# Optimization experiments

Measured on AMD Instinct MI355X. Metric: run time of the kernel, lower is better.

The kernel has to match this reference:

```python
import jax, jax.numpy as jnp
import numpy as np

# Module constants (from init_kwargs)
D_MODEL = 128
N_HEADS = 8
D_H = D_MODEL // N_HEADS
SCALE = D_H ** -0.5
D_IN = 8          # number of channels
SEQ_LEN = 128     # per-channel key length (S = D_IN*SEQ_LEN)


def setup_inputs() -> dict:
    key = jax.random.key(0)
    ks = jax.random.split(key, 16)
    B, P, S = 8, 512, 1024
    Q = jax.random.normal(ks[0], (B, P, D_MODEL), jnp.float32)
    K = jax.random.normal(ks[1], (B, S, D_MODEL), jnp.float32)
    V = jax.random.normal(ks[2], (B, S, D_MODEL), jnp.float32)
    prev = jax.random.normal(ks[3], (B, P, N_HEADS, S), jnp.float32)
    # cross-channel mask: attend only to tokens from a *different* channel
    pred_ch = jnp.arange(P) // (P // D_IN)          # (P,)
    seq_ch = jnp.arange(S) // SEQ_LEN               # (S,)
    attn_mask = (pred_ch[:, None] != seq_ch[None, :]).reshape(1, P, 1, S)
    w = lambda k, shp: jax.random.normal(k, shp, jnp.float32) * 0.02
    Wq, bq = w(ks[4], (D_MODEL, D_MODEL)), w(ks[5], (D_MODEL,))
    Wk, bk = w(ks[6], (D_MODEL, D_MODEL)), w(ks[7], (D_MODEL,))
    Wv, bv = w(ks[8], (D_MODEL, D_MODEL)), w(ks[9], (D_MODEL,))
    Wo, bo = w(ks[10], (D_MODEL, D_MODEL)), w(ks[11], (D_MODEL,))
    ch_gate = jax.random.normal(ks[12], (D_IN, D_IN), jnp.float32)
    return dict(Q=Q, K=K, V=V, prev=prev, attn_mask=attn_mask,
                Wq=Wq, bq=bq, Wk=Wk, bk=bk, Wv=Wv, bv=bv, Wo=Wo, bo=bo,
                ch_gate=ch_gate)


def reference(Q, K, V, prev, attn_mask, Wq, bq, Wk, bk, Wv, bv, Wo, bo, ch_gate):
    B, P, _ = Q.shape
    S = K.shape[1]
    H, dh = N_HEADS, D_H
    q = (Q @ Wq.T + bq).reshape(B, P, H, dh)
    k = (K @ Wk.T + bk).reshape(B, S, H, dh)
    v = (V @ Wv.T + bv).reshape(B, S, H, dh)
    raw_scores = jnp.einsum('bphd,bshd->bphs', q, k) * SCALE
    raw_scores = raw_scores + prev                     # residual attention
    # channel gating with STE
    pred_ch = jnp.arange(P) // (P // D_IN)
    seq_ch = jnp.arange(S) // SEQ_LEN
    s = jax.nn.sigmoid(ch_gate)
    hard = (s >= 0.5).astype(s.dtype)
    gate_ch = hard + (s - jax.lax.stop_gradient(s))
    gate_full = gate_ch[pred_ch][:, seq_ch].reshape(1, P, 1, S)
    raw_scores = jnp.where(jnp.isfinite(raw_scores), raw_scores * gate_full, raw_scores)
    # stable masked softmax with explicit renormalization
    stable = raw_scores - jnp.max(raw_scores, axis=-1, keepdims=True)
    masked = jnp.where(attn_mask, stable, -1e9)
    attn = jax.nn.softmax(masked, axis=-1)
    attn = attn * attn_mask.astype(attn.dtype)
    den = jnp.clip(jnp.sum(attn, axis=-1, keepdims=True), 1e-9, None)
    attn = attn / den
    out = jnp.einsum('bphs,bshd->bphd', attn, v).reshape(B, P, H * dh)
    out = out @ Wo.T + bo
    return out, attn, raw_scores
```

## Files before the change

kernel.cpp:

```cpp
#include <hip/hip_runtime.h>
#include <hip/hip_bf16.h>

typedef unsigned short u16;
typedef float f32x4 __attribute__((ext_vector_type(4)));
typedef __bf16 bf16x8 __attribute__((ext_vector_type(8)));
typedef _Float16 f16x8 __attribute__((ext_vector_type(8)));
typedef _Float16 f16x2 __attribute__((ext_vector_type(2)));

union Frag { int4 i; bf16x8 b; f16x8 h; };

__device__ inline u16 f2bf(float f) {
  union { float f; unsigned u; } v; v.f = f;
  unsigned r = v.u + 0x7FFFu + ((v.u >> 16) & 1u);
  return (u16)(r >> 16);
}
__device__ inline unsigned pk_f16(float a, float b) {
  return __builtin_bit_cast(unsigned, __builtin_amdgcn_cvt_pkrtz(a, b));
}

__device__ __forceinline__ void lds_barrier() {
  asm volatile("s_waitcnt lgkmcnt(0)" ::: "memory");
  __builtin_amdgcn_s_barrier();
}

__device__ __forceinline__
void proj_body(u16* __restrict__ smem,
               const float* __restrict__ X, const float* __restrict__ W,
               const float* __restrict__ bias, void* __restrict__ out,
               int mode, int innerShift, int rows0)
{
  u16* XL = smem;
  u16* WL = smem + 64 * 136;

  const int tid = threadIdx.x;
  const int w = tid >> 6, l = tid & 63, lg = l >> 4, lr = l & 15;

  #pragma unroll
  for (int i = 0; i < 8; ++i) {
    int u = tid + i * 256;
    int rr = u >> 5, c4 = (u & 31) * 4;
    const float4 xv = *(const float4*)(X + (rows0 + rr) * 128 + c4);
    uint2 p;
    p.x = (unsigned)f2bf(xv.x) | ((unsigned)f2bf(xv.y) << 16);
    p.y = (unsigned)f2bf(xv.z) | ((unsigned)f2bf(xv.w) << 16);
    *(uint2*)(XL + rr * 136 + c4) = p;
  }
  #pragma unroll
  for (int i = 0; i < 16; ++i) {
    int u = tid + i * 256;
    int rr = u >> 5, c4 = (u & 31) * 4;
    const float4 xv = *(const float4*)(W + rr * 128 + c4);
    uint2 p;
    p.x = (unsigned)f2bf(xv.x) | ((unsigned)f2bf(xv.y) << 16);
    p.y = (unsigned)f2bf(xv.z) | ((unsigned)f2bf(xv.w) << 16);
    *(uint2*)(WL + rr * 136 + c4) = p;
  }
  __syncthreads();

  Frag a[4];
  #pragma unroll
  for (int kc = 0; kc < 4; ++kc)
    a[kc].i = *(const int4*)(XL + (16 * w + lr) * 136 + kc * 32 + 8 * lg);

  f32x4 acc[8];
  #pragma unroll
  for (int ct = 0; ct < 8; ++ct) {
    f32x4 c = {0.f, 0.f, 0.f, 0.f};
    #pragma unroll
    for (int kc = 0; kc < 4; ++kc) {
      Frag bw;
      bw.i = *(const int4*)(WL + (ct * 16 + lr) * 136 + kc * 32 + 8 * lg);
      c = __builtin_amdgcn_mfma_f32_16x16x32_bf16(a[kc].b, bw.b, c, 0, 0, 0);
    }
    acc[ct] = c;
  }

  if (mode == 2) {
    float* o = (float*)out;
    #pragma unroll
    for (int ct = 0; ct < 8; ++ct) {
      float bn = bias[ct * 16 + lr];
      #pragma unroll
      for (int j = 0; j < 4; ++j) {
        int row = rows0 + 16 * w + 4 * lg + j;
        o[row * 128 + ct * 16 + lr] = acc[ct][j] + bn;
      }
    }
  } else if (mode == 0) {
    u16* o = (u16*)out;
    const int innerMask = (1 << innerShift) - 1;
    #pragma unroll
    for (int ct = 0; ct < 8; ++ct) {
      float bn = bias[ct * 16 + lr];
      #pragma unroll
      for (int j = 0; j < 4; ++j) {
        int row = rows0 + 16 * w + 4 * lg + j;
        int bI = row >> innerShift, r = row & innerMask;
        o[(((bI * 8 + ct) << innerShift) + r) * 16 + lr] =
            __builtin_bit_cast(u16, (_Float16)(acc[ct][j] + bn));
      }
    }
  } else {
    __syncthreads();
    u16* YT = smem;
    #pragma unroll
    for (int ct = 0; ct < 8; ++ct) {
      float bn = bias[ct * 16 + lr];
      #pragma unroll
      for (int j = 0; j < 4; ++j)
        YT[(ct * 16 + lr) * 72 + 16 * w + 4 * lg + j] =
            __builtin_bit_cast(u16, (_Float16)(acc[ct][j] + bn));
    }
    __syncthreads();
    u16* o = (u16*)out;
    const int bI = rows0 >> 10, s0 = rows0 & 1023;
    #pragma unroll
    for (int i = 0; i < 4; ++i) {
      int u = tid + i * 256;
      int n = u >> 3, ch = (u & 7) * 8;
      int4 v = *(const int4*)(YT + n * 72 + ch);
      *(int4*)(o + ((bI * 8 + (n >> 4)) * 16 + (n & 15)) * 1024 + s0 + ch) = v;
    }
  }
}

__global__ __launch_bounds__(256, 2)
void proj_qkv(const float* __restrict__ Q, const float* __restrict__ K,
              const float* __restrict__ V,
              const float* __restrict__ Wq, const float* __restrict__ bq,
              const float* __restrict__ Wk, const float* __restrict__ bk,
              const float* __restrict__ Wv, const float* __restrict__ bv,
              u16* __restrict__ qb, u16* __restrict__ kb, u16* __restrict__ vtb)
{
  __shared__ __attribute__((aligned(16))) u16 smem[26112];
  const int bid = blockIdx.x;
  if (bid < 64)       proj_body(smem, Q, Wq, bq, qb,  0,  9, bid * 64);
  else if (bid < 192) proj_body(smem, K, Wk, bk, kb,  0, 10, (bid - 64) * 64);
  else                proj_body(smem, V, Wv, bv, vtb, 1, 10, (bid - 192) * 64);
}

__global__ __launch_bounds__(256, 2)
void proj_out(const float* __restrict__ X, const float* __restrict__ W,
              const float* __restrict__ bias, float* __restrict__ out)
{
  __shared__ __attribute__((aligned(16))) u16 smem[26112];
  proj_body(smem, X, W, bias, out, 2, 9, blockIdx.x * 64);
}

__device__ __forceinline__ int swz(int row, int elem) {
  return row * 1024 + (elem ^ ((row & 7) << 3));
}

__global__ __launch_bounds__(256, 5)
void attn_kernel(const u16* __restrict__ qb, const u16* __restrict__ kb,
                 const u16* __restrict__ vtb, const float* __restrict__ prev,
                 const float* __restrict__ ch_gate,
                 float* __restrict__ rs_out, float* __restrict__ attn_out,
                 float* __restrict__ preout)
{
  __shared__ __attribute__((aligned(16))) u16 SRS[16384];

  const int bid = blockIdx.x;
  const int vb = (bid & 7) * 256 + (bid >> 3);
  const int pt = vb & 31, h = (vb >> 5) & 7, b = vb >> 8;
  const int p0 = pt * 16, ptch = pt >> 2;
  const int tid = threadIdx.x, w = tid >> 6, l = tid & 63;
  const int lg = l >> 4, lr = l & 15;

  unsigned gbits = 0u;
  #pragma unroll
  for (int j = 0; j < 8; ++j)
    if (ch_gate[ptch * 8 + j] >= 0.f) gbits |= (1u << j);
  gbits = __builtin_amdgcn_readfirstlane(gbits);

  const int r = 4 * w + lg;
  const int base = ((b * 512 + p0) * 8 + h) * 1024;
  const float* prow = prev + base + r * 8192;
  float* rsrow = rs_out + base + r * 8192;
  float* arow  = attn_out + base + r * 8192;

  const f32x4 zf = {0.f, 0.f, 0.f, 0.f};
  f32x4 pf0 = (gbits & 1u) ? __builtin_nontemporal_load((const f32x4*)(prow +   0 + lr * 4)) : zf;
  f32x4 pf1 = (gbits & 1u) ? __builtin_nontemporal_load((const f32x4*)(prow +  64 + lr * 4)) : zf;
  f32x4 pf2 = (gbits & 2u) ? __builtin_nontemporal_load((const f32x4*)(prow + 128 + lr * 4)) : zf;
  f32x4 pf3 = (gbits & 2u) ? __builtin_nontemporal_load((const f32x4*)(prow + 192 + lr * 4)) : zf;
  f32x4 pf4 = (gbits & 4u) ? __builtin_nontemporal_load((const f32x4*)(prow + 256 + lr * 4)) : zf;
  f32x4 pf5 = (gbits & 4u) ? __builtin_nontemporal_load((const f32x4*)(prow + 320 + lr * 4)) : zf;

  float den = 0.f;
  uint2 eh[16];
  #pragma unroll
  for (int it = 0; it < 16; ++it) {
    const int ch = it >> 1;
    const int s = it * 64 + lr * 4;
    if (!((gbits >> ch) & 1u)) {
      __builtin_nontemporal_store(zf, (f32x4*)(rsrow + s));
      if (ch == ptch) eh[it] = make_uint2(0u, 0u);
      else          { eh[it] = make_uint2(0x3C003C00u, 0x3C003C00u); den += 4.f; }
      *(uint2*)&SRS[swz(r, s)] = eh[it];
    }
    if (ch == ptch)
      __builtin_nontemporal_store(zf, (f32x4*)(arow + s));
  }

  Frag aq;
  if (lg < 2) aq.i = *(const int4*)(qb + (((b * 8 + h) * 512 + p0 + lr) * 16 + 8 * lg));
  else        aq.i = make_int4(0, 0, 0, 0);

  const u16* kbase = kb + (b * 8 + h) * 1024 * 16;
  const int sbase = w * 256;

  #pragma unroll 2
  for (int st = 0; st < 16; ++st) {
    const int s0 = sbase + st * 16;
    if (!((gbits >> (s0 >> 7)) & 1u)) continue;
    Frag bk;
    if (lg < 2) bk.i = *(const int4*)(kbase + (s0 + lr) * 16 + 8 * lg);
    else        bk.i = make_int4(0, 0, 0, 0);
    f32x4 zero = {0.f, 0.f, 0.f, 0.f};
    f32x4 d = __builtin_amdgcn_mfma_f32_16x16x32_f16(bk.h, aq.h, zero, 0, 0, 0);
    uint2 pk2;
    pk2.x = pk_f16(d[0] * 0.25f, d[1] * 0.25f);
    pk2.y = pk_f16(d[2] * 0.25f, d[3] * 0.25f);
    *(uint2*)&SRS[swz(lr, s0 + 4 * lg)] = pk2;
  }
  lds_barrier();

  #pragma unroll
  for (int it = 0; it < 16; ++it) {
    const int ch = it >> 1;
    if (!((gbits >> ch) & 1u)) continue;
    const int s = it * 64 + lr * 4;
    const bool msk = (ch == ptch);
    f32x4 pv;
    if      (it == 0) pv = pf0;
    else if (it == 1) pv = pf1;
    else if (it == 2) pv = pf2;
    else if (it == 3) pv = pf3;
    else if (it == 4) pv = pf4;
    else if (it == 5) pv = pf5;
    else pv = __builtin_nontemporal_load((const f32x4*)(prow + s));
    union { uint2 u; f16x2 hh[2]; } sc;
    sc.u = *(const uint2*)&SRS[swz(r, s)];
    f32x4 rs;
    rs[0] = (float)sc.hh[0][0] + pv[0];
    rs[1] = (float)sc.hh[0][1] + pv[1];
    rs[2] = (float)sc.hh[1][0] + pv[2];
    rs[3] = (float)sc.hh[1][1] + pv[3];
    __builtin_nontemporal_store(rs, (f32x4*)(rsrow + s));
    if (msk) {
      eh[it] = make_uint2(0u, 0u);
    } else {
      float e0 = __expf(rs[0]);
      float e1 = __expf(rs[1]);
      float e2 = __expf(rs[2]);
      float e3 = __expf(rs[3]);
      den += (e0 + e1) + (e2 + e3);
      eh[it].x = pk_f16(e0, e1);
      eh[it].y = pk_f16(e2, e3);
    }
    *(uint2*)&SRS[swz(r, s)] = eh[it];
  }

  #pragma unroll
  for (int off = 1; off < 16; off <<= 1)
    den += __shfl_xor(den, off);
  const float invd = 1.f / den;
  lds_barrier();

  f32x4 acc = {0.f, 0.f, 0.f, 0.f};
  const u16* vbase = vtb + ((b * 8 + h) * 16 + lr) * 1024;
  #pragma unroll
  for (int kc = 0; kc < 8; ++kc) {
    Frag pa, bv;
    pa.i = *(const int4*)(&SRS[swz(lr, sbase + kc * 32 + 8 * lg)]);
    bv.i = *(const int4*)(vbase + sbase + kc * 32 + 8 * lg);
    acc = __builtin_amdgcn_mfma_f32_16x16x32_f16(pa.h, bv.h, acc, 0, 0, 0);
  }

  lds_barrier();
  {
    float* OutBuf = (float*)SRS;
    #pragma unroll
    for (int j = 0; j < 4; ++j)
      OutBuf[(w * 16 + 4 * lg + j) * 20 + lr] = acc[j];
    if (lr == 0) OutBuf[1280 + r] = invd;
  }
  lds_barrier();
  {
    float* OutBuf = (float*)SRS;
    const int pr = tid >> 4, dd = tid & 15;
    float o = (OutBuf[pr * 20 + dd] + OutBuf[(16 + pr) * 20 + dd] +
               OutBuf[(32 + pr) * 20 + dd] + OutBuf[(48 + pr) * 20 + dd]) *
              OutBuf[1280 + pr];
    preout[((b * 512 + p0 + pr) * 8 + h) * 16 + dd] = o;
  }

  {
    #pragma unroll
    for (int it = 0; it < 16; ++it) {
      const int ch = it >> 1;
      if (ch == ptch) continue;
      const int s = it * 64 + lr * 4;
      union { uint2 u; f16x2 hh[2]; } e;
      e.u = eh[it];
      f32x4 o;
      o[0] = (float)e.hh[0][0] * invd;
      o[1] = (float)e.hh[0][1] * invd;
      o[2] = (float)e.hh[1][0] * invd;
      o[3] = (float)e.hh[1][1] * invd;
      __builtin_nontemporal_store(o, (f32x4*)(arow + s));
    }
  }
}

extern "C" void kernel_launch(void* const* d_in, const int* in_sizes, int n_in,
                              void* d_out, int out_size, void* d_ws, size_t ws_size,
                              hipStream_t stream)
{
  (void)in_sizes; (void)n_in; (void)out_size; (void)ws_size;
  const float* Q       = (const float*)d_in[0];
  const float* K       = (const float*)d_in[1];
  const float* V       = (const float*)d_in[2];
  const float* prev    = (const float*)d_in[3];
  const float* Wq      = (const float*)d_in[5];
  const float* bq      = (const float*)d_in[6];
  const float* Wk      = (const float*)d_in[7];
  const float* bk      = (const float*)d_in[8];
  const float* Wv      = (const float*)d_in[9];
  const float* bv      = (const float*)d_in[10];
  const float* Wo      = (const float*)d_in[11];
  const float* bo      = (const float*)d_in[12];
  const float* ch_gate = (const float*)d_in[13];

  u16*   qb     = (u16*)d_ws;
  u16*   kb     = qb + 524288;
  u16*   vtb    = kb + 1048576;
  float* preout = (float*)((char*)d_ws + 5242880);

  float* outp     = (float*)d_out;
  float* attn_out = outp + 524288;
  float* rs_out   = outp + 34078720;

  proj_qkv<<<320, 256, 0, stream>>>(Q, K, V, Wq, bq, Wk, bk, Wv, bv,
                                    qb, kb, vtb);
  attn_kernel<<<2048, 256, 0, stream>>>(qb, kb, vtb, prev, ch_gate,
                                        rs_out, attn_out, preout);
  proj_out<<<64, 256, 0, stream>>>(preout, Wo, bo, outp);
}
```

Baseline: 98.49 us.

## Split output projection across column tiles and use regular stores for attention outputs

The output projection becomes its own kernel. Each block computes 64 rows by 32 output columns, so the launch grows from 64 to 256 blocks and the small GEMM uses more of the GPU. Separately, the attention kernel's large fp32 writes to raw_scores and attn change from nontemporal stores to ordinary stores. The second change alters cache behaviour for roughly 270MB of output writes, which could help or hurt write bandwidth.

```diff
diff --git a/kernel.cpp b/kernel.cpp
--- a/kernel.cpp
+++ b/kernel.cpp
@@ -75,18 +75,7 @@
     acc[ct] = c;
   }
 
-  if (mode == 2) {
-    float* o = (float*)out;
-    #pragma unroll
-    for (int ct = 0; ct < 8; ++ct) {
-      float bn = bias[ct * 16 + lr];
-      #pragma unroll
-      for (int j = 0; j < 4; ++j) {
-        int row = rows0 + 16 * w + 4 * lg + j;
-        o[row * 128 + ct * 16 + lr] = acc[ct][j] + bn;
-      }
-    }
-  } else if (mode == 0) {
+  if (mode == 0) {
     u16* o = (u16*)out;
     const int innerMask = (1 << innerShift) - 1;
     #pragma unroll
@@ -140,11 +129,61 @@
 }
 
 __global__ __launch_bounds__(256, 2)
-void proj_out(const float* __restrict__ X, const float* __restrict__ W,
-              const float* __restrict__ bias, float* __restrict__ out)
-{
-  __shared__ __attribute__((aligned(16))) u16 smem[26112];
-  proj_body(smem, X, W, bias, out, 2, 9, blockIdx.x * 64);
+void proj_out_kernel(const float* __restrict__ X, const float* __restrict__ W,
+                     const float* __restrict__ bias, float* __restrict__ out)
+{
+  __shared__ __attribute__((aligned(16))) u16 smem[13056];
+  u16* XL = smem;
+  u16* WL = smem + 64 * 136;
+
+  const int tid = threadIdx.x;
+  const int w = tid >> 6, l = tid & 63, lg = l >> 4, lr = l & 15;
+  const int rows0 = (blockIdx.x >> 2) * 64;
+  const int c0 = (blockIdx.x & 3) * 32;
+
+  #pragma unroll
+  for (int i = 0; i < 8; ++i) {
+    int u = tid + i * 256;
+    int rr = u >> 5, c4 = (u & 31) * 4;
+    const float4 xv = *(const float4*)(X + (rows0 + rr) * 128 + c4);
+    uint2 p;
+    p.x = (unsigned)f2bf(xv.x) | ((unsigned)f2bf(xv.y) << 16);
+    p.y = (unsigned)f2bf(xv.z) | ((unsigned)f2bf(xv.w) << 16);
+    *(uint2*)(XL + rr * 136 + c4) = p;
+  }
+  #pragma unroll
+  for (int i = 0; i < 4; ++i) {
+    int u = tid + i * 256;
+    int rr = u >> 5, c4 = (u & 31) * 4;
+    const float4 xv = *(const float4*)(W + (c0 + rr) * 128 + c4);
+    uint2 p;
+    p.x = (unsigned)f2bf(xv.x) | ((unsigned)f2bf(xv.y) << 16);
+    p.y = (unsigned)f2bf(xv.z) | ((unsigned)f2bf(xv.w) << 16);
+    *(uint2*)(WL + rr * 136 + c4) = p;
+  }
+  __syncthreads();
+
+  Frag a[4];
+  #pragma unroll
+  for (int kc = 0; kc < 4; ++kc)
+    a[kc].i = *(const int4*)(XL + (16 * w + lr) * 136 + kc * 32 + 8 * lg);
+
+  #pragma unroll
+  for (int ct = 0; ct < 2; ++ct) {
+    f32x4 c = {0.f, 0.f, 0.f, 0.f};
+    #pragma unroll
+    for (int kc = 0; kc < 4; ++kc) {
+      Frag bw;
+      bw.i = *(const int4*)(WL + (ct * 16 + lr) * 136 + kc * 32 + 8 * lg);
+      c = __builtin_amdgcn_mfma_f32_16x16x32_bf16(a[kc].b, bw.b, c, 0, 0, 0);
+    }
+    float bn = bias[c0 + ct * 16 + lr];
+    #pragma unroll
+    for (int j = 0; j < 4; ++j) {
+      int row = rows0 + 16 * w + 4 * lg + j;
+      out[row * 128 + c0 + ct * 16 + lr] = c[j] + bn;
+    }
+  }
 }
 
 __device__ __forceinline__ int swz(int row, int elem) {
@@ -194,13 +233,13 @@
     const int ch = it >> 1;
     const int s = it * 64 + lr * 4;
     if (!((gbits >> ch) & 1u)) {
-      __builtin_nontemporal_store(zf, (f32x4*)(rsrow + s));
+      *(f32x4*)(rsrow + s) = zf;
       if (ch == ptch) eh[it] = make_uint2(0u, 0u);
       else          { eh[it] = make_uint2(0x3C003C00u, 0x3C003C00u); den += 4.f; }
       *(uint2*)&SRS[swz(r, s)] = eh[it];
     }
     if (ch == ptch)
-      __builtin_nontemporal_store(zf, (f32x4*)(arow + s));
+      *(f32x4*)(arow + s) = zf;
   }
 
   Frag aq;
@@ -247,7 +286,7 @@
     rs[1] = (float)sc.hh[0][1] + pv[1];
     rs[2] = (float)sc.hh[1][0] + pv[2];
     rs[3] = (float)sc.hh[1][1] + pv[3];
-    __builtin_nontemporal_store(rs, (f32x4*)(rsrow + s));
+    *(f32x4*)(rsrow + s) = rs;
     if (msk) {
       eh[it] = make_uint2(0u, 0u);
     } else {
@@ -309,7 +348,7 @@
       o[1] = (float)e.hh[0][1] * invd;
       o[2] = (float)e.hh[1][0] * invd;
       o[3] = (float)e.hh[1][1] * invd;
-      __builtin_nontemporal_store(o, (f32x4*)(arow + s));
+      *(f32x4*)(arow + s) = o;
     }
   }
 }
@@ -346,5 +385,5 @@
                                     qb, kb, vtb);
   attn_kernel<<<2048, 256, 0, stream>>>(qb, kb, vtb, prev, ch_gate,
                                         rs_out, attn_out, preout);
-  proj_out<<<64, 256, 0, stream>>>(preout, Wo, bo, outp);
-}
+  proj_out_kernel<<<256, 256, 0, stream>>>(preout, Wo, bo, outp);
+}
```

Result: faster. 87.36 us, median of 2 (-11.3%).
